# Optimization experiments

Measured on AMD Instinct MI355X. Metric: run time of the kernel, lower is better.

Reference implementation:

```python
import jax, jax.numpy as jnp
import numpy as np

N, E = 10000, 320000
IN, HID, HEADS, OUT = 1280, 128, 4, 500
NEG_SLOPE = 0.2
BN_EPS = 1e-5


def gat_layer(x, src, dst, W, a_src, a_dst, b, concat):
    """PyG-style GATConv (single weight matrix, additive attention, scatter-softmax)."""
    n = x.shape[0]
    H, C = a_src.shape
    xp = (x @ W).reshape(n, H, C)                      # [N,H,C]
    s = jnp.sum(xp * a_src, axis=-1)                   # [N,H] src attention logits
    d = jnp.sum(xp * a_dst, axis=-1)                   # [N,H] dst attention logits
    e = jax.nn.leaky_relu(s[src] + d[dst], NEG_SLOPE)  # [Etot,H]
    # scatter-softmax over edges sharing the same destination node
    m = jax.ops.segment_max(e, dst, num_segments=n)
    ex = jnp.exp(e - m[dst])
    z = jax.ops.segment_sum(ex, dst, num_segments=n)
    alpha = ex / z[dst]                                # [Etot,H]
    out = jax.ops.segment_sum(alpha[:, :, None] * xp[src], dst, num_segments=n)  # [N,H,C]
    out = out.reshape(n, H * C) if concat else out.mean(axis=1)
    return out + b


def batch_norm(x, gamma, beta):
    mu = x.mean(axis=0)
    var = x.var(axis=0)  # biased, matches torch BN training normalization
    return (x - mu) * jax.lax.rsqrt(var + BN_EPS) * gamma + beta


def setup_inputs() -> dict:
    key = jax.random.key(0)
    ks = jax.random.split(key, 20)
    rn = lambda k, shape, s=0.05: jax.random.normal(k, shape, jnp.float32) * s
    HC = HID * HEADS
    return {
        "x": jax.random.normal(ks[0], (N, IN), jnp.float32),
        "edge_index": jax.random.randint(ks[1], (2, E), 0, N, jnp.int64 if jax.config.jax_enable_x64 else jnp.int32),
        "W1": rn(ks[2], (IN, HC)), "a_src1": rn(ks[3], (HEADS, HID)), "a_dst1": rn(ks[4], (HEADS, HID)), "b1": jnp.zeros((HC,), jnp.float32),
        "g1": jnp.ones((HC,), jnp.float32), "be1": jnp.zeros((HC,), jnp.float32),
        "W2": rn(ks[5], (HC, HC)), "a_src2": rn(ks[6], (HEADS, HID)), "a_dst2": rn(ks[7], (HEADS, HID)), "b2": jnp.zeros((HC,), jnp.float32),
        "g2": jnp.ones((HC,), jnp.float32), "be2": jnp.zeros((HC,), jnp.float32),
        "W3": rn(ks[8], (HC, OUT)), "a_src3": rn(ks[9], (1, OUT)), "a_dst3": rn(ks[10], (1, OUT)), "b3": jnp.zeros((OUT,), jnp.float32),
    }


def reference(x, edge_index, W1, a_src1, a_dst1, b1, g1, be1,
              W2, a_src2, a_dst2, b2, g2, be2, W3, a_src3, a_dst3, b3):
    n = x.shape[0]
    loops = jnp.arange(n, dtype=edge_index.dtype)
    src = jnp.concatenate([edge_index[0], loops])  # PyG add_self_loops=True
    dst = jnp.concatenate([edge_index[1], loops])
    h = gat_layer(x, src, dst, W1, a_src1, a_dst1, b1, concat=True)
    h = jax.nn.elu(batch_norm(h, g1, be1))
    h = gat_layer(h, src, dst, W2, a_src2, a_dst2, b2, concat=True)
    h = jax.nn.elu(batch_norm(h, g2, be2))
    return gat_layer(h, src, dst, W3, a_src3, a_dst3, b3, concat=False)
```

## Files before the change

### kernel.cpp

```cpp
#include <hip/hip_runtime.h>
#include <hip/hip_bf16.h>

#define NNODES 10000
#define NEDGES 320000
#define INF_   1280
#define HID_   128
#define HEADS_ 4
#define OUTF_  500
#define HC_    512
#define NEG_SLOPE 0.2f
#define BN_EPS 1e-5f

typedef __attribute__((ext_vector_type(8))) short short8x;
typedef __attribute__((ext_vector_type(4))) float f32x4;
typedef unsigned short ushort_t;
typedef unsigned int uint_t;

__device__ __forceinline__ ushort_t f2bf(float f) {
    uint_t u = __float_as_uint(f);
    u = (u + 0x7fffu + ((u >> 16) & 1u)) >> 16;
    return (ushort_t)u;
}
__device__ __forceinline__ float bf_lo(uint_t p) { return __uint_as_float(p << 16); }
__device__ __forceinline__ float bf_hi(uint_t p) { return __uint_as_float(p & 0xffff0000u); }
__device__ __forceinline__ float lrelu(float x) { return (x >= 0.f) ? x : NEG_SLOPE * x; }
__device__ __forceinline__ float eluf(float x) { return (x > 0.f) ? x : (__expf(x) - 1.0f); }
__device__ __forceinline__ uint_t pack_bf16_rn(float a, float b) {
    __hip_bfloat162 h = __float22bfloat162_rn(make_float2(a, b));
    return *(uint_t*)&h;
}

#define CVX (NNODES * INF_ / 4)
#define CN1 (HC_ * INF_)
#define CN2 (HC_ * HC_)
#define CN3 (HC_ * HC_)
#define CZC (NNODES / 4)
#define CZ3 (NNODES / 2)
__global__ void convall_kernel(const float* __restrict__ x,
                               const float* __restrict__ W1,
                               const float* __restrict__ W2,
                               const float* __restrict__ W3,
                               ushort_t* __restrict__ x_bf,
                               ushort_t* __restrict__ Wt1,
                               ushort_t* __restrict__ Wt2,
                               ushort_t* __restrict__ Wt3,
                               uint4* __restrict__ zc,
                               uint4* __restrict__ zz) {
    int i = blockIdx.x * blockDim.x + threadIdx.x;
    if (i < CVX) {
        float4 v = ((const float4*)x)[i];
        ((uint2*)x_bf)[i] = make_uint2(pack_bf16_rn(v.x, v.y), pack_bf16_rn(v.z, v.w));
    } else if (i < CVX + CN1) {
        int j = i - CVX;
        int n = j / INF_, k = j - n * INF_;
        Wt1[j] = f2bf(W1[(size_t)k * HC_ + n]);
    } else if (i < CVX + CN1 + CN2) {
        int j = i - CVX - CN1;
        int n = j / HC_, k = j - n * HC_;
        Wt2[j] = f2bf(W2[(size_t)k * HC_ + n]);
    } else if (i < CVX + CN1 + CN2 + CN3) {
        int j = i - CVX - CN1 - CN2;
        int n = j / HC_, k = j - n * HC_;
        Wt3[j] = (n < OUTF_) ? f2bf(W3[(size_t)k * OUTF_ + n]) : (ushort_t)0;
    } else if (i < CVX + CN1 + CN2 + CN3 + CZC) {
        zc[i - CVX - CN1 - CN2 - CN3] = make_uint4(0, 0, 0, 0);
    } else if (i < CVX + CN1 + CN2 + CN3 + CZC + CZ3) {
        zz[i - CVX - CN1 - CN2 - CN3 - CZC] = make_uint4(0, 0, 0, 0);
    }
}

__global__ void count_kernel(const int* __restrict__ dst, int* __restrict__ counts, int E) {
    int e = blockIdx.x * blockDim.x + threadIdx.x;
    if (e < E) atomicAdd(&counts[dst[e]], 1);
}

__global__ __launch_bounds__(1024) void scan_fused_kernel(const int* __restrict__ counts,
                                                          int* __restrict__ offsets,
                                                          int* __restrict__ cursor, int n) {
    __shared__ int wsum[16];
    int t = threadIdx.x;
    int lane = t & 63, wv = t >> 6;
    int base = t * 10;
    int v[10];
    int s = 0;
#pragma unroll
    for (int k = 0; k < 10; ++k) {
        int i = base + k;
        int c = (i < n) ? counts[i] : 0;
        v[k] = s;
        s += c;
    }
    int incl = s;
#pragma unroll
    for (int off = 1; off < 64; off <<= 1) {
        int u = __shfl_up(incl, off, 64);
        if (lane >= off) incl += u;
    }
    if (lane == 63) wsum[wv] = incl;
    __syncthreads();
    if (t < 16) {
        int ws = wsum[t];
        int in2 = ws;
#pragma unroll
        for (int off = 1; off < 16; off <<= 1) {
            int u = __shfl_up(in2, off, 64);
            if (t >= off) in2 += u;
        }
        wsum[t] = in2 - ws;
    }
    __syncthreads();
    int basep = wsum[wv] + (incl - s);
#pragma unroll
    for (int k = 0; k < 10; ++k) {
        int i = base + k;
        if (i < n) {
            int o = basep + v[k];
            offsets[i] = o;
            cursor[i] = o;
        }
    }
    if (t == 1023) offsets[n] = basep + s;
}

__global__ void scatter_kernel(const int* __restrict__ src, const int* __restrict__ dst,
                               int* __restrict__ cursor, int* __restrict__ esrc, int E) {
    int e = blockIdx.x * blockDim.x + threadIdx.x;
    if (e < E) {
        int p = atomicAdd(&cursor[dst[e]], 1);
        esrc[p] = src[e];
    }
}

#define LDT 40

template<int LOGIT, bool BNA>
__global__ __launch_bounds__(256) void gemm_kernel(
    const void* __restrict__ Ain,
    const ushort_t* __restrict__ Bt,
    ushort_t* __restrict__ Cb,
    const float* __restrict__ bnsc,
    const float* __restrict__ bnsh,
    const float* __restrict__ aS,
    const float* __restrict__ aD,
    float* __restrict__ s_log,
    float* __restrict__ d_log,
    int M, int K)
{
    __shared__ __align__(16) ushort_t As[64 * LDT];
    __shared__ __align__(16) ushort_t Bs[128 * LDT];
    __shared__ float sred[64][2], dred[64][2];

    int nblk = gridDim.x;
    int orig = blockIdx.x;
    int q = nblk >> 3, r = nblk & 7;
    int xcd = orig & 7;
    int lid = (xcd < r ? xcd * (q + 1) : r * (q + 1) + (xcd - r) * q) + (orig >> 3);
    int m0 = (lid >> 2) * 64;
    int n0 = (lid & 3) * 128;

    int tid  = threadIdx.x;
    int lane = tid & 63;
    int w    = tid >> 6;
    int wm   = (w & 1) * 32;
    int wn   = (w >> 1) * 64;
    int quad = lane >> 4;
    int c16  = lane & 15;

    f32x4 acc[2][4];
#pragma unroll
    for (int i = 0; i < 2; ++i)
#pragma unroll
        for (int j = 0; j < 4; ++j)
#pragma unroll
            for (int r2 = 0; r2 < 4; ++r2) acc[i][j][r2] = 0.0f;

    int sr = tid >> 2;
    int sk = (tid & 3) * 8;
    int gm = m0 + sr;  if (gm > M - 1) gm = M - 1;
    const ushort_t* aptr  = nullptr;
    const float*    aptrf = nullptr;
    if (BNA) aptrf = (const float*)Ain + (size_t)gm * K + sk;
    else     aptr  = (const ushort_t*)Ain + (size_t)gm * K + sk;
    int br0 = tid >> 2;
    int bk0 = (tid & 3) * 8;
    int br1 = (256 + tid) >> 2;
    int bk1 = bk0;
    const ushort_t* bptr0 = Bt + (size_t)(n0 + br0) * K + bk0;
    const ushort_t* bptr1 = Bt + (size_t)(n0 + br1) * K + bk1;

    uint4 av_a, av_b;
    float4 fa0_a, fa1_a, fa0_b, fa1_b;
    if (BNA) {
        fa0_a = *(const float4*)(aptrf);
        fa1_a = *(const float4*)(aptrf + 4);
        if (K > 32) {
            fa0_b = *(const float4*)(aptrf + 32);
            fa1_b = *(const float4*)(aptrf + 36);
        }
    } else {
        av_a = *(const uint4*)(aptr);
        if (K > 32) av_b = *(const uint4*)(aptr + 32);
    }
    uint4 bv0_a = *(const uint4*)(bptr0);
    uint4 bv1_a = *(const uint4*)(bptr1);
    uint4 bv0_b, bv1_b;
    if (K > 32) {
        bv0_b = *(const uint4*)(bptr0 + 32);
        bv1_b = *(const uint4*)(bptr1 + 32);
    }

    for (int k0 = 0; k0 < K; k0 += 32) {
        if (BNA) {
            int cb = k0 + sk;
            float4 sc0 = *(const float4*)(bnsc + cb);
            float4 sc1 = *(const float4*)(bnsc + cb + 4);
            float4 sh0 = *(const float4*)(bnsh + cb);
            float4 sh1 = *(const float4*)(bnsh + cb + 4);
            float v0 = eluf(fa0_a.x * sc0.x + sh0.x);
            float v1 = eluf(fa0_a.y * sc0.y + sh0.y);
            float v2 = eluf(fa0_a.z * sc0.z + sh0.z);
            float v3 = eluf(fa0_a.w * sc0.w + sh0.w);
            float v4 = eluf(fa1_a.x * sc1.x + sh1.x);
            float v5 = eluf(fa1_a.y * sc1.y + sh1.y);
            float v6 = eluf(fa1_a.z * sc1.z + sh1.z);
            float v7 = eluf(fa1_a.w * sc1.w + sh1.w);
            *(uint4*)&As[sr * LDT + sk] = make_uint4(
                pack_bf16_rn(v0, v1), pack_bf16_rn(v2, v3),
                pack_bf16_rn(v4, v5), pack_bf16_rn(v6, v7));
        } else {
            *(uint4*)&As[sr * LDT + sk] = av_a;
        }
        *(uint4*)&Bs[br0 * LDT + bk0] = bv0_a;
        *(uint4*)&Bs[br1 * LDT + bk1] = bv1_a;
        __syncthreads();

        short8x af0 = *(const short8x*)&As[(wm +      c16) * LDT + quad * 8];
        short8x af1 = *(const short8x*)&As[(wm + 16 + c16) * LDT + quad * 8];
        short8x bf[4];
#pragma unroll
        for (int nt = 0; nt < 4; ++nt)
            bf[nt] = *(const short8x*)&Bs[(wn + nt * 16 + c16) * LDT + quad * 8];

        if (BNA) {
            fa0_a = fa0_b; fa1_a = fa1_b;
            if (k0 + 64 < K) {
                fa0_b = *(const float4*)(aptrf + k0 + 64);
                fa1_b = *(const float4*)(aptrf + k0 + 68);
            }
        } else {
            av_a = av_b;
            if (k0 + 64 < K) av_b = *(const uint4*)(aptr + k0 + 64);
        }
        bv0_a = bv0_b; bv1_a = bv1_b;
        if (k0 + 64 < K) {
            bv0_b = *(const uint4*)(bptr0 + k0 + 64);
            bv1_b = *(const uint4*)(bptr1 + k0 + 64);
        }

#pragma unroll
        for (int nt = 0; nt < 4; ++nt) {
            acc[0][nt] = __builtin_amdgcn_mfma_f32_16x16x32_bf16(af0, bf[nt], acc[0][nt], 0, 0, 0);
            acc[1][nt] = __builtin_amdgcn_mfma_f32_16x16x32_bf16(af1, bf[nt], acc[1][nt], 0, 0, 0);
        }
        __syncthreads();
    }

#pragma unroll
    for (int mt = 0; mt < 2; ++mt) {
#pragma unroll
        for (int r2 = 0; r2 < 4; ++r2) {
            int row = m0 + wm + mt * 16 + quad * 4 + r2;
            if (row < M) {
#pragma unroll
                for (int nt = 0; nt < 4; ++nt) {
                    int col = n0 + wn + nt * 16 + c16;
                    Cb[(size_t)row * 512 + col] = f2bf(acc[mt][nt][r2]);
                }
            }
        }
    }

    float as_[4], ad_[4];
#pragma unroll
    for (int nt = 0; nt < 4; ++nt) {
        int colg = n0 + wn + nt * 16 + c16;
        if (LOGIT == 4) {
            as_[nt] = aS[colg];
            ad_[nt] = aD[colg];
        } else {
            as_[nt] = (colg < OUTF_) ? aS[colg] : 0.f;
            ad_[nt] = (colg < OUTF_) ? aD[colg] : 0.f;
        }
    }
#pragma unroll
    for (int mt = 0; mt < 2; ++mt) {
#pragma unroll
        for (int r2 = 0; r2 < 4; ++r2) {
            float ps = acc[mt][0][r2] * as_[0] + acc[mt][1][r2] * as_[1]
                     + acc[mt][2][r2] * as_[2] + acc[mt][3][r2] * as_[3];
            float pd = acc[mt][0][r2] * ad_[0] + acc[mt][1][r2] * ad_[1]
                     + acc[mt][2][r2] * ad_[2] + acc[mt][3][r2] * ad_[3];
#pragma unroll
            for (int off = 1; off < 16; off <<= 1) {
                ps += __shfl_xor(ps, off);
                pd += __shfl_xor(pd, off);
            }
            if (c16 == 0) {
                int rl = wm + mt * 16 + quad * 4 + r2;
                sred[rl][wn >> 6] = ps;
                dred[rl][wn >> 6] = pd;
            }
        }
    }
    __syncthreads();
    if (tid < 64) {
        int row = m0 + tid;
        if (row < M) {
            float s = sred[tid][0] + sred[tid][1];
            float d = dred[tid][0] + dred[tid][1];
            if (LOGIT == 4) {
                int h = n0 >> 7;
                s_log[row * 4 + h] = s;
                d_log[row * 4 + h] = d;
            } else {
                atomicAdd(&s_log[row], s);
                atomicAdd(&d_log[row], d);
            }
        }
    }
}

__device__ __forceinline__ void acc8(float* acc, uint4 q, float w) {
    acc[0] += w * bf_lo(q.x); acc[1] += w * bf_hi(q.x);
    acc[2] += w * bf_lo(q.y); acc[3] += w * bf_hi(q.y);
    acc[4] += w * bf_lo(q.z); acc[5] += w * bf_hi(q.z);
    acc[6] += w * bf_lo(q.w); acc[7] += w * bf_hi(q.w);
}

template<int H>
__global__ __launch_bounds__(256) void gather_fused_kernel(
    const uint4* __restrict__ xpb4,
    const int* __restrict__ offsets, const int* __restrict__ esrc,
    const float* __restrict__ s_log,
    const float* __restrict__ d_log,
    const float* __restrict__ bias,
    float* __restrict__ out,
    int OUTC, int ldo)
{
    int id = blockIdx.x;
    int xcd = id & 7;
    int slice = xcd >> 1;
    int sub2 = xcd & 1;
    int wv = threadIdx.x >> 6;
    int node = (id >> 3) * 8 + sub2 * 4 + wv;
    if (node >= NNODES) return;
    int lane = threadIdx.x & 63;
    int esub = lane >> 4;
    int l16 = lane & 15;
    int h = (H == 4) ? slice : 0;
    int rowoff = slice * 16 + l16;

    float dh = d_log[node * H + h];
    float c0 = lrelu(s_log[node * H + h] + dh);

    float acc[8];
    float z;
    if (esub == 0) {
        uint4 p = xpb4[(size_t)node * 64 + rowoff];
        acc[0] = bf_lo(p.x); acc[1] = bf_hi(p.x);
        acc[2] = bf_lo(p.y); acc[3] = bf_hi(p.y);
        acc[4] = bf_lo(p.z); acc[5] = bf_hi(p.z);
        acc[6] = bf_lo(p.w); acc[7] = bf_hi(p.w);
        z = 1.0f;
    } else {
#pragma unroll
        for (int k = 0; k < 8; ++k) acc[k] = 0.f;
        z = 0.f;
    }

    int e0 = offsets[node], e1 = offsets[node + 1];
    int j = e0 + esub;
    for (; j + 12 < e1; j += 16) {
        int s0 = esrc[j], s1 = esrc[j + 4], s2 = esrc[j + 8], s3 = esrc[j + 12];
        uint4 q0 = xpb4[(size_t)s0 * 64 + rowoff];
        uint4 q1 = xpb4[(size_t)s1 * 64 + rowoff];
        uint4 q2 = xpb4[(size_t)s2 * 64 + rowoff];
        uint4 q3 = xpb4[(size_t)s3 * 64 + rowoff];
        float w0 = __expf(lrelu(s_log[s0 * H + h] + dh) - c0);
        float w1 = __expf(lrelu(s_log[s1 * H + h] + dh) - c0);
        float w2 = __expf(lrelu(s_log[s2 * H + h] + dh) - c0);
        float w3 = __expf(lrelu(s_log[s3 * H + h] + dh) - c0);
        acc8(acc, q0, w0);
        acc8(acc, q1, w1);
        acc8(acc, q2, w2);
        acc8(acc, q3, w3);
        z += w0 + w1 + w2 + w3;
    }
    for (; j < e1; j += 4) {
        int s0 = esrc[j];
        uint4 q0 = xpb4[(size_t)s0 * 64 + rowoff];
        float w0 = __expf(lrelu(s_log[s0 * H + h] + dh) - c0);
        acc8(acc, q0, w0);
        z += w0;
    }

#pragma unroll
    for (int k = 0; k < 8; ++k) {
        acc[k] += __shfl_xor(acc[k], 16);
        acc[k] += __shfl_xor(acc[k], 32);
    }
    z += __shfl_xor(z, 16);
    z += __shfl_xor(z, 32);

    if (esub == 0) {
        float zi = 1.0f / z;
        int cbase = slice * 128 + l16 * 8;
        size_t ob = (size_t)node * ldo + cbase;
        if (cbase + 7 < OUTC) {
            float4 o0 = make_float4(acc[0] * zi + bias[cbase + 0], acc[1] * zi + bias[cbase + 1],
                                    acc[2] * zi + bias[cbase + 2], acc[3] * zi + bias[cbase + 3]);
            float4 o1 = make_float4(acc[4] * zi + bias[cbase + 4], acc[5] * zi + bias[cbase + 5],
                                    acc[6] * zi + bias[cbase + 6], acc[7] * zi + bias[cbase + 7]);
            *(float4*)(out + ob) = o0;
            *(float4*)(out + ob + 4) = o1;
        } else {
#pragma unroll
            for (int k = 0; k < 8; ++k) {
                int c = cbase + k;
                if (c < OUTC) out[ob + k] = acc[k] * zi + bias[c];
            }
        }
    }
}

#define BNB 256

__global__ __launch_bounds__(512) void bn_stats_kernel(const float* __restrict__ h,
                                                       float* __restrict__ psum,
                                                       float* __restrict__ psumsq) {
    int c = threadIdx.x;
    int b = blockIdx.x;
    float sm = 0.f, sq = 0.f;
#pragma unroll 4
    for (int r2 = b; r2 < NNODES; r2 += BNB) {
        float v = h[(size_t)r2 * 512 + c];
        sm += v;
        sq += v * v;
    }
    psum[b * 512 + c] = sm;
    psumsq[b * 512 + c] = sq;
}

__global__ __launch_bounds__(512) void bn_finalize_kernel(const float* __restrict__ psum,
                                                          const float* __restrict__ psumsq,
                                                          const float* __restrict__ gamma,
                                                          const float* __restrict__ beta,
                                                          float* __restrict__ scale,
                                                          float* __restrict__ shift) {
    int t = threadIdx.x;
    int wv = t >> 6, lane = t & 63;
    int c = blockIdx.x * 8 + wv;
    float s = 0.f, q = 0.f;
#pragma unroll
    for (int k = 0; k < BNB / 64; ++k) {
        int b = lane + k * 64;
        s += psum[b * 512 + c];
        q += psumsq[b * 512 + c];
    }
#pragma unroll
    for (int off = 32; off > 0; off >>= 1) {
        s += __shfl_xor(s, off);
        q += __shfl_xor(q, off);
    }
    if (lane == 0) {
        const float invN = 1.0f / (float)NNODES;
        float mu = s * invN;
        float var = q * invN - mu * mu;
        float sc = gamma[c] * rsqrtf(var + BN_EPS);
        scale[c] = sc;
        shift[c] = beta[c] - mu * sc;
    }
}

extern "C" void kernel_launch(void* const* d_in, const int* in_sizes, int n_in,
                              void* d_out, int out_size, void* d_ws, size_t ws_size,
                              hipStream_t stream) {
    const float* x      = (const float*)d_in[0];
    const int*   ei     = (const int*)d_in[1];
    const float* W1     = (const float*)d_in[2];
    const float* a_src1 = (const float*)d_in[3];
    const float* a_dst1 = (const float*)d_in[4];
    const float* b1     = (const float*)d_in[5];
    const float* g1     = (const float*)d_in[6];
    const float* be1    = (const float*)d_in[7];
    const float* W2     = (const float*)d_in[8];
    const float* a_src2 = (const float*)d_in[9];
    const float* a_dst2 = (const float*)d_in[10];
    const float* b2     = (const float*)d_in[11];
    const float* g2     = (const float*)d_in[12];
    const float* be2    = (const float*)d_in[13];
    const float* W3     = (const float*)d_in[14];
    const float* a_src3 = (const float*)d_in[15];
    const float* a_dst3 = (const float*)d_in[16];
    const float* b3     = (const float*)d_in[17];
    float* out = (float*)d_out;

    const int* e_src = ei;
    const int* e_dst = ei + NEDGES;

    char* w = (char*)d_ws;
    ushort_t* x_bf = (ushort_t*)w;
    float*    hbuf = (float*)w;
    w += (size_t)NNODES * INF_ * sizeof(ushort_t);
    uint_t* xpb = (uint_t*)w;  w += (size_t)NNODES * HC_ * sizeof(ushort_t);
    ushort_t* Wt1 = (ushort_t*)w; w += (size_t)HC_ * INF_ * sizeof(ushort_t);
    ushort_t* Wt2 = (ushort_t*)w; w += (size_t)HC_ * HC_ * sizeof(ushort_t);
    ushort_t* Wt3 = (ushort_t*)w; w += (size_t)HC_ * HC_ * sizeof(ushort_t);
    int* counts  = (int*)w;    w += NNODES * sizeof(int);
    float* s_log = (float*)w;  w += NNODES * HEADS_ * sizeof(float);
    float* d_log = (float*)w;  w += NNODES * HEADS_ * sizeof(float);
    float* s3_log = (float*)w; w += NNODES * sizeof(float);
    float* d3_log = (float*)w; w += NNODES * sizeof(float);
    float* bnscale = (float*)w; w += HC_ * sizeof(float);
    float* bnshift = (float*)w; w += HC_ * sizeof(float);
    float* psum  = (float*)w;  w += (size_t)BNB * HC_ * sizeof(float);
    float* psumsq= (float*)w;  w += (size_t)BNB * HC_ * sizeof(float);
    int* offsets = (int*)w;    w += (NNODES + 1) * sizeof(int);
    int* cursor  = (int*)w;    w += NNODES * sizeof(int);
    int* esrc    = (int*)w;    w += NEDGES * sizeof(int);

    const int ggBlocks = (HC_ / 128) * ((NNODES + 63) / 64);
    const int gaGrid = ((NNODES + 7) / 8) * 8;

    {
        int TOT = CVX + CN1 + CN2 + CN3 + CZC + CZ3;
        convall_kernel<<<(TOT + 255) / 256, 256, 0, stream>>>(x, W1, W2, W3,
            x_bf, Wt1, Wt2, Wt3, (uint4*)counts, (uint4*)s3_log);
    }
    count_kernel<<<(NEDGES + 255) / 256, 256, 0, stream>>>(e_dst, counts, NEDGES);
    scan_fused_kernel<<<1, 1024, 0, stream>>>(counts, offsets, cursor, NNODES);
    scatter_kernel<<<(NEDGES + 255) / 256, 256, 0, stream>>>(e_src, e_dst, cursor, esrc, NEDGES);

    gemm_kernel<4, false><<<ggBlocks, 256, 0, stream>>>(x_bf, Wt1, (ushort_t*)xpb,
        nullptr, nullptr, a_src1, a_dst1, s_log, d_log, NNODES, INF_);
    gather_fused_kernel<HEADS_><<<gaGrid, 256, 0, stream>>>((const uint4*)xpb, offsets, esrc,
        s_log, d_log, b1, hbuf, HC_, HC_);
    bn_stats_kernel<<<BNB, 512, 0, stream>>>(hbuf, psum, psumsq);
    bn_finalize_kernel<<<64, 512, 0, stream>>>(psum, psumsq, g1, be1, bnscale, bnshift);

    gemm_kernel<4, true><<<ggBlocks, 256, 0, stream>>>(hbuf, Wt2, (ushort_t*)xpb,
        bnscale, bnshift, a_src2, a_dst2, s_log, d_log, NNODES, HC_);
    gather_fused_kernel<HEADS_><<<gaGrid, 256, 0, stream>>>((const uint4*)xpb, offsets, esrc,
        s_log, d_log, b2, hbuf, HC_, HC_);
    bn_stats_kernel<<<BNB, 512, 0, stream>>>(hbuf, psum, psumsq);
    bn_finalize_kernel<<<64, 512, 0, stream>>>(psum, psumsq, g2, be2, bnscale, bnshift);

    gemm_kernel<1, true><<<ggBlocks, 256, 0, stream>>>(hbuf, Wt3, (ushort_t*)xpb,
        bnscale, bnshift, a_src3, a_dst3, s3_log, d3_log, NNODES, HC_);
    gather_fused_kernel<1><<<gaGrid, 256, 0, stream>>>((const uint4*)xpb, offsets, esrc,
        s3_log, d3_log, b3, out, OUTF_, OUTF_);
}
```

Before: 383.1 us.

## Fuse batch-norm statistics accumulation into the attention gather kernel

The gather kernel now writes per-block partial sums and sums of squares of its output via shared memory, replacing the separate bn_stats pass over the hidden activations. The finalize kernel reduces over the per-block banks instead of a fixed count. This removes a full re-read of the activation matrix per layer, but adds a block barrier to the gather and makes finalize read a much larger partial-sum array with only 64 blocks.

```diff
diff --git a/kernel.cpp b/kernel.cpp
--- a/kernel.cpp
+++ b/kernel.cpp
@@ -330,6 +330,8 @@
     }
 }
 
+#define GBANKS (2 * ((NNODES + 7) / 8))
+
 __device__ __forceinline__ void acc8(float* acc, uint4 q, float w) {
     acc[0] += w * bf_lo(q.x); acc[1] += w * bf_hi(q.x);
     acc[2] += w * bf_lo(q.y); acc[3] += w * bf_hi(q.y);
@@ -337,7 +339,7 @@
     acc[6] += w * bf_lo(q.w); acc[7] += w * bf_hi(q.w);
 }
 
-template<int H>
+template<int H, bool BN>
 __global__ __launch_bounds__(256) void gather_fused_kernel(
     const uint4* __restrict__ xpb4,
     const int* __restrict__ offsets, const int* __restrict__ esrc,
@@ -345,27 +347,33 @@
     const float* __restrict__ d_log,
     const float* __restrict__ bias,
     float* __restrict__ out,
+    float* __restrict__ psum,
+    float* __restrict__ psumsq,
     int OUTC, int ldo)
 {
+    __shared__ float vsh[4][128];
+    __shared__ float vsqh[4][128];
+
     int id = blockIdx.x;
     int xcd = id & 7;
     int slice = xcd >> 1;
     int sub2 = xcd & 1;
     int wv = threadIdx.x >> 6;
     int node = (id >> 3) * 8 + sub2 * 4 + wv;
-    if (node >= NNODES) return;
+    bool valid = node < NNODES;
+    if (!BN && !valid) return;
     int lane = threadIdx.x & 63;
     int esub = lane >> 4;
     int l16 = lane & 15;
     int h = (H == 4) ? slice : 0;
     int rowoff = slice * 16 + l16;
 
-    float dh = d_log[node * H + h];
-    float c0 = lrelu(s_log[node * H + h] + dh);
+    float dh = valid ? d_log[node * H + h] : 0.f;
+    float c0 = valid ? lrelu(s_log[node * H + h] + dh) : 0.f;
 
     float acc[8];
     float z;
-    if (esub == 0) {
+    if (esub == 0 && valid) {
         uint4 p = xpb4[(size_t)node * 64 + rowoff];
         acc[0] = bf_lo(p.x); acc[1] = bf_hi(p.x);
         acc[2] = bf_lo(p.y); acc[3] = bf_hi(p.y);
@@ -378,7 +386,8 @@
         z = 0.f;
     }
 
-    int e0 = offsets[node], e1 = offsets[node + 1];
+    int e0 = valid ? offsets[node] : 0;
+    int e1 = valid ? offsets[node + 1] : 0;
     int j = e0 + esub;
     for (; j + 12 < e1; j += 16) {
         int s0 = esrc[j], s1 = esrc[j + 4], s2 = esrc[j + 8], s3 = esrc[j + 12];
@@ -416,39 +425,42 @@
         float zi = 1.0f / z;
         int cbase = slice * 128 + l16 * 8;
         size_t ob = (size_t)node * ldo + cbase;
-        if (cbase + 7 < OUTC) {
-            float4 o0 = make_float4(acc[0] * zi + bias[cbase + 0], acc[1] * zi + bias[cbase + 1],
-                                    acc[2] * zi + bias[cbase + 2], acc[3] * zi + bias[cbase + 3]);
-            float4 o1 = make_float4(acc[4] * zi + bias[cbase + 4], acc[5] * zi + bias[cbase + 5],
-                                    acc[6] * zi + bias[cbase + 6], acc[7] * zi + bias[cbase + 7]);
-            *(float4*)(out + ob) = o0;
-            *(float4*)(out + ob + 4) = o1;
-        } else {
+        float v[8];
+#pragma unroll
+        for (int k = 0; k < 8; ++k) v[k] = acc[k] * zi + bias[(cbase + k < 512) ? cbase + k : 0];
+        if (valid) {
+            if (cbase + 7 < OUTC) {
+                *(float4*)(out + ob)     = make_float4(v[0], v[1], v[2], v[3]);
+                *(float4*)(out + ob + 4) = make_float4(v[4], v[5], v[6], v[7]);
+            } else {
+#pragma unroll
+                for (int k = 0; k < 8; ++k) {
+                    int c = cbase + k;
+                    if (c < OUTC) out[ob + k] = v[k];
+                }
+            }
+        }
+        if (BN) {
 #pragma unroll
             for (int k = 0; k < 8; ++k) {
-                int c = cbase + k;
-                if (c < OUTC) out[ob + k] = acc[k] * zi + bias[c];
-            }
-        }
-    }
-}
-
-#define BNB 256
-
-__global__ __launch_bounds__(512) void bn_stats_kernel(const float* __restrict__ h,
-                                                       float* __restrict__ psum,
-                                                       float* __restrict__ psumsq) {
-    int c = threadIdx.x;
-    int b = blockIdx.x;
-    float sm = 0.f, sq = 0.f;
-#pragma unroll 4
-    for (int r2 = b; r2 < NNODES; r2 += BNB) {
-        float v = h[(size_t)r2 * 512 + c];
-        sm += v;
-        sq += v * v;
-    }
-    psum[b * 512 + c] = sm;
-    psumsq[b * 512 + c] = sq;
+                float vv = valid ? v[k] : 0.f;
+                vsh[wv][l16 * 8 + k] = vv;
+                vsqh[wv][l16 * 8 + k] = vv * vv;
+            }
+        }
+    }
+    if (BN) {
+        __syncthreads();
+        int t = threadIdx.x;
+        if (t < 128) {
+            float s = vsh[0][t] + vsh[1][t] + vsh[2][t] + vsh[3][t];
+            float q = vsqh[0][t] + vsqh[1][t] + vsqh[2][t] + vsqh[3][t];
+            int bank = (id >> 3) * 2 + sub2;
+            size_t off = (size_t)bank * 512 + slice * 128 + t;
+            psum[off] = s;
+            psumsq[off] = q;
+        }
+    }
 }
 
 __global__ __launch_bounds__(512) void bn_finalize_kernel(const float* __restrict__ psum,
@@ -461,11 +473,10 @@
     int wv = t >> 6, lane = t & 63;
     int c = blockIdx.x * 8 + wv;
     float s = 0.f, q = 0.f;
-#pragma unroll
-    for (int k = 0; k < BNB / 64; ++k) {
-        int b = lane + k * 64;
-        s += psum[b * 512 + c];
-        q += psumsq[b * 512 + c];
+#pragma unroll 4
+    for (int b = lane; b < GBANKS; b += 64) {
+        s += psum[(size_t)b * 512 + c];
+        q += psumsq[(size_t)b * 512 + c];
     }
 #pragma unroll
     for (int off = 32; off > 0; off >>= 1) {
@@ -523,8 +534,8 @@
     float* d3_log = (float*)w; w += NNODES * sizeof(float);
     float* bnscale = (float*)w; w += HC_ * sizeof(float);
     float* bnshift = (float*)w; w += HC_ * sizeof(float);
-    float* psum  = (float*)w;  w += (size_t)BNB * HC_ * sizeof(float);
-    float* psumsq= (float*)w;  w += (size_t)BNB * HC_ * sizeof(float);
+    float* psum  = (float*)w;  w += (size_t)GBANKS * HC_ * sizeof(float);
+    float* psumsq= (float*)w;  w += (size_t)GBANKS * HC_ * sizeof(float);
     int* offsets = (int*)w;    w += (NNODES + 1) * sizeof(int);
     int* cursor  = (int*)w;    w += NNODES * sizeof(int);
     int* esrc    = (int*)w;    w += NEDGES * sizeof(int);
@@ -543,20 +554,18 @@
 
     gemm_kernel<4, false><<<ggBlocks, 256, 0, stream>>>(x_bf, Wt1, (ushort_t*)xpb,
         nullptr, nullptr, a_src1, a_dst1, s_log, d_log, NNODES, INF_);
-    gather_fused_kernel<HEADS_><<<gaGrid, 256, 0, stream>>>((const uint4*)xpb, offsets, esrc,
-        s_log, d_log, b1, hbuf, HC_, HC_);
-    bn_stats_kernel<<<BNB, 512, 0, stream>>>(hbuf, psum, psumsq);
+    gather_fused_kernel<HEADS_, true><<<gaGrid, 256, 0, stream>>>((const uint4*)xpb, offsets, esrc,
+        s_log, d_log, b1, hbuf, psum, psumsq, HC_, HC_);
     bn_finalize_kernel<<<64, 512, 0, stream>>>(psum, psumsq, g1, be1, bnscale, bnshift);
 
     gemm_kernel<4, true><<<ggBlocks, 256, 0, stream>>>(hbuf, Wt2, (ushort_t*)xpb,
         bnscale, bnshift, a_src2, a_dst2, s_log, d_log, NNODES, HC_);
-    gather_fused_kernel<HEADS_><<<gaGrid, 256, 0, stream>>>((const uint4*)xpb, offsets, esrc,
-        s_log, d_log, b2, hbuf, HC_, HC_);
-    bn_stats_kernel<<<BNB, 512, 0, stream>>>(hbuf, psum, psumsq);
+    gather_fused_kernel<HEADS_, true><<<gaGrid, 256, 0, stream>>>((const uint4*)xpb, offsets, esrc,
+        s_log, d_log, b2, hbuf, psum, psumsq, HC_, HC_);
     bn_finalize_kernel<<<64, 512, 0, stream>>>(psum, psumsq, g2, be2, bnscale, bnshift);
 
     gemm_kernel<1, true><<<ggBlocks, 256, 0, stream>>>(hbuf, Wt3, (ushort_t*)xpb,
         bnscale, bnshift, a_src3, a_dst3, s3_log, d3_log, NNODES, HC_);
-    gather_fused_kernel<1><<<gaGrid, 256, 0, stream>>>((const uint4*)xpb, offsets, esrc,
-        s3_log, d3_log, b3, out, OUTF_, OUTF_);
-}
+    gather_fused_kernel<1, false><<<gaGrid, 256, 0, stream>>>((const uint4*)xpb, offsets, esrc,
+        s3_log, d3_log, b3, out, nullptr, nullptr, OUTF_, OUTF_);
+}
```

After: 435.9 us. +13.8%, slower.
